# Performance work log

Hardware: AMD Instinct MI355X
Metric: run time of the kernel (lower is better)

Reference implementation:

```python
import jax, jax.numpy as jnp
import numpy as np
import math

B, S, D, H, F = 4, 1024, 1024, 16, 4096
NUM_BUCKETS, MAX_DISTANCE = 32, 128
LN_EPS = 1e-5


def _relative_position_bucket(relative_position, num_buckets=NUM_BUCKETS, max_distance=MAX_DISTANCE):
    # bidirectional T5 bucketing, faithful to the torch source
    n = -relative_position
    num_buckets = num_buckets // 2  # 16
    ret = (n < 0).astype(jnp.int32) * num_buckets
    n = jnp.abs(n)
    max_exact = num_buckets // 2  # 8
    is_small = n < max_exact
    val_if_large = max_exact + (
        jnp.log(jnp.maximum(n, 1).astype(jnp.float32) / max_exact)
        / math.log(max_distance / max_exact)
        * (num_buckets - max_exact)
    ).astype(jnp.int32)
    val_if_large = jnp.minimum(val_if_large, num_buckets - 1)
    return ret + jnp.where(is_small, n, val_if_large)


def layer_norm(x, g, b):
    mu = jnp.mean(x, axis=-1, keepdims=True)
    var = jnp.mean((x - mu) ** 2, axis=-1, keepdims=True)
    return g * (x - mu) / jnp.sqrt(var + LN_EPS) + b


def setup_inputs() -> dict:
    key = jax.random.key(0)
    ks = jax.random.split(key, 12)
    s = 0.02
    return {
        "in_state": jax.random.normal(ks[0], (B, S, D), jnp.float32),
        "padding_mask": jnp.ones((B, S), jnp.int32),
        "Wq": jax.random.normal(ks[1], (D, D), jnp.float32) * s,
        "bq": jnp.zeros((D,), jnp.float32),
        "Wk": jax.random.normal(ks[2], (D, D), jnp.float32) * s,
        "bk": jnp.zeros((D,), jnp.float32),
        "Wv": jax.random.normal(ks[3], (D, D), jnp.float32) * s,
        "bv": jnp.zeros((D,), jnp.float32),
        "Wo": jax.random.normal(ks[4], (D, D), jnp.float32) * s,
        "bo": jnp.zeros((D,), jnp.float32),
        "rel_bias": jax.random.normal(ks[5], (NUM_BUCKETS, H), jnp.float32) * s,
        "ln1_g": jnp.ones((D,), jnp.float32),
        "ln1_b": jnp.zeros((D,), jnp.float32),
        "W1": jax.random.normal(ks[6], (D, F), jnp.float32) * s,
        "b1": jnp.zeros((F,), jnp.float32),
        "W2": jax.random.normal(ks[7], (F, D), jnp.float32) * s,
        "b2": jnp.zeros((D,), jnp.float32),
        "ln2_g": jnp.ones((D,), jnp.float32),
        "ln2_b": jnp.zeros((D,), jnp.float32),
    }


def reference(in_state, padding_mask, Wq, bq, Wk, bk, Wv, bv, Wo, bo, rel_bias,
              ln1_g, ln1_b, W1, b1, W2, b2, ln2_g, ln2_b):
    b, s, d = in_state.shape
    dh = d // H
    q = in_state @ Wq + bq
    k = in_state @ Wk + bk
    v = in_state @ Wv + bv
    # faithful to torch's q.view(B*H, S, d_head) flat reshape (no head transpose)
    qh = q.reshape(b * H, s, dh)
    kh = k.reshape(b * H, s, dh)
    vh = v.reshape(b * H, s, dh)
    scores = jnp.einsum('bqd,bkd->bqk', qh, kh)  # no 1/sqrt(d) scaling (T5 style)
    # relative position bias: [H, S, S] tiled over batch -> block index b*H+h gets head h
    rel_pos = jnp.arange(s)[:, None] - jnp.arange(s)[None, :]
    buckets = _relative_position_bucket(rel_pos)
    bias = rel_bias[buckets].transpose(2, 0, 1)  # [H, S, S]
    bias = jnp.tile(bias, (b, 1, 1))  # [B*H, S, S]
    # padding mask: log(0/1) -> -inf/0; block b*H+h uses mask[b, value_index]
    pad = jnp.log(padding_mask.astype(jnp.float32))  # [B, S]
    pad = jnp.repeat(pad, H, axis=0)[:, None, :]  # [B*H, 1, S]
    attw = jax.nn.softmax(scores + bias + pad, axis=-1)
    att = (attw @ vh).reshape(b, s, d)
    att = att @ Wo + bo
    h = layer_norm(att + in_state, ln1_g, ln1_b)
    ff = jnp.maximum(h @ W1 + b1, 0.0) @ W2 + b2
    out = layer_norm(ff + h, ln2_g, ln2_b)
    return out
```

## Files before the change

### kernel.cpp

```cpp
#include <hip/hip_runtime.h>
#include <hip/hip_bf16.h>

typedef unsigned short u16;
typedef __attribute__((ext_vector_type(8))) short bhalf8;
typedef __attribute__((ext_vector_type(4))) float f32x4;

#define DEV __device__ __forceinline__

DEV float bf2f(u16 u) { union { unsigned int i; float f; } c; c.i = ((unsigned int)u) << 16; return c.f; }
DEV u16 f2bf(float f) {
  union { float f; unsigned int i; } c; c.f = f;
  unsigned int x = c.i;
  x += 0x7fffu + ((x >> 16) & 1u);
  return (u16)(x >> 16);
}

DEV void async16(const void* g, void* l) {
  __builtin_amdgcn_global_load_lds((__attribute__((address_space(1))) void*)g,
                                   (__attribute__((address_space(3))) void*)l, 16, 0, 0);
}

struct Ptr11 { const void* p[11]; };
struct TC4 { const void* in[4]; u16* out[4]; };

__global__ void detect_kernel(const unsigned int* __restrict__ x, int* __restrict__ flag) {
  int t = threadIdx.x;
  int cnt = 0;
  for (int i = t; i < 256; i += 64) {
    unsigned int w = x[i];
    int e = (w >> 7) & 0xFF;
    if (e >= 96 && e <= 134) cnt++;
  }
#pragma unroll
  for (int o = 1; o < 64; o <<= 1) cnt += __shfl_xor(cnt, o, 64);
  if (t == 0) *flag = (cnt >= 192) ? 1 : 0;
}

DEV bhalf8 load8B(const void* base, size_t e, int isbf) {
  if (isbf) return *(const bhalf8*)((const u16*)base + e);
  const float* f = (const float*)base + e;
  float4 a = *(const float4*)f;
  float4 b = *(const float4*)(f + 4);
  bhalf8 r;
  r[0] = (short)f2bf(a.x); r[1] = (short)f2bf(a.y); r[2] = (short)f2bf(a.z); r[3] = (short)f2bf(a.w);
  r[4] = (short)f2bf(b.x); r[5] = (short)f2bf(b.y); r[6] = (short)f2bf(b.z); r[7] = (short)f2bf(b.w);
  return r;
}

__global__ __launch_bounds__(256) void convert_x(const void* __restrict__ x,
                                                 u16* __restrict__ dst,
                                                 const int* __restrict__ flag) {
  int c = blockIdx.x * 256 + threadIdx.x;
  u16* d = dst + (size_t)c * 4;
  if (*flag) {
    *(ushort4*)d = ((const ushort4*)x)[c];
  } else {
    float4 v = ((const float4*)x)[c];
    d[0] = f2bf(v.x); d[1] = f2bf(v.y); d[2] = f2bf(v.z); d[3] = f2bf(v.w);
  }
}

__global__ __launch_bounds__(256) void convert_small(Ptr11 s, float* __restrict__ dst,
                                                     const int* __restrict__ flag) {
  const int isbf = *flag;
  const int SZ[11] = {1024,1024,1024,1024,512,1024,1024,4096,1024,1024,1024};
  for (int i = threadIdx.x; i < 13824; i += 256) {
    int acc = 0, seg = -1, off = 0;
#pragma unroll
    for (int s2 = 0; s2 < 11; ++s2) {
      if (seg < 0 && i < acc + SZ[s2]) { seg = s2; off = i - acc; }
      acc += SZ[s2];
    }
    dst[i] = isbf ? bf2f(((const u16*)s.p[seg])[off]) : ((const float*)s.p[seg])[off];
  }
}

DEV void tconv_tile(const void* in, u16* out, int R, int C, int isbf) {
  __shared__ __align__(16) u16 tile[64][72];
  const int t = threadIdx.x;
  const int c0 = blockIdx.x * 64, r0 = blockIdx.y * 64;
#pragma unroll
  for (int r = 0; r < 2; ++r) {
    int idx = r * 256 + t;
    int ri = idx >> 3, cc = (idx & 7) * 8;
    bhalf8 v = load8B(in, (size_t)(r0 + ri) * C + c0 + cc, isbf);
    *(bhalf8*)(&tile[ri][cc]) = v;
  }
  __syncthreads();
#pragma unroll
  for (int r = 0; r < 2; ++r) {
    int idx = r * 256 + t;
    int co = idx >> 3, rc = (idx & 7) * 8;
    bhalf8 v;
#pragma unroll
    for (int ii = 0; ii < 8; ++ii) v[ii] = (short)tile[rc + ii][co];
    *(bhalf8*)(out + (size_t)(c0 + co) * R + r0 + rc) = v;
  }
}

__global__ __launch_bounds__(256) void tconv_w4(TC4 p, const int* __restrict__ flag) {
  int z = blockIdx.z;
  tconv_tile(p.in[z], p.out[z], 1024, 1024, *flag);
}

__global__ __launch_bounds__(256) void tconv_generic(const void* in, u16* out, int R, int C,
                                                     const int* __restrict__ flag) {
  tconv_tile(in, out, R, C, *flag);
}

__global__ __launch_bounds__(256) void transpose_generic(const u16* in, u16* out, int R, int C) {
  __shared__ __align__(16) u16 tile[64][72];
  const int t = threadIdx.x;
  const int c0 = blockIdx.x * 64, r0 = blockIdx.y * 64;
  size_t bs = (size_t)R * C * blockIdx.z;
#pragma unroll
  for (int r = 0; r < 2; ++r) {
    int idx = r * 256 + t;
    int ri = idx >> 3, cc = (idx & 7) * 8;
    *(bhalf8*)(&tile[ri][cc]) = *(const bhalf8*)(in + bs + (size_t)(r0 + ri) * C + c0 + cc);
  }
  __syncthreads();
#pragma unroll
  for (int r = 0; r < 2; ++r) {
    int idx = r * 256 + t;
    int co = idx >> 3, rc = (idx & 7) * 8;
    bhalf8 v;
#pragma unroll
    for (int ii = 0; ii < 8; ++ii) v[ii] = (short)tile[rc + ii][co];
    *(bhalf8*)(out + bs + (size_t)(c0 + co) * R + r0 + rc) = v;
  }
}

template<int BN, int RELU>
__global__ __launch_bounds__(256) void gemm_bt(
    const u16* __restrict__ A, const u16* __restrict__ BT0,
    const float* __restrict__ b0, const float* __restrict__ b1, const float* __restrict__ b2,
    u16* __restrict__ C0, int M, int N, int K, long sBT, long sC)
{
  constexpr int NFRAG = BN / 32;
  constexpr int BSLOT = BN * 4 / 256;
  __shared__ __align__(16) u16 ldsA[128 * 32];
  __shared__ __align__(16) u16 ldsB[BN * 32];

  const int t = threadIdx.x;
  const int wv = t >> 6, l = t & 63;
  const int wm = wv & 1, wn = wv >> 1;
  const int m0 = blockIdx.y * 128, n0 = blockIdx.x * BN;
  const int z = blockIdx.z;

  const u16* BT = BT0 + (long)z * sBT;
  const float* bias = (z == 0) ? b0 : (z == 1 ? b1 : b2);
  u16* C = C0 + (long)z * sC;

  const u16* agp[2];
#pragma unroll
  for (int r = 0; r < 2; ++r) {
    int s = r * 256 + t;
    int mm = s >> 2, c = (s & 3) ^ ((s >> 4) & 3);
    agp[r] = A + (size_t)(m0 + mm) * K + c * 8;
  }
  const u16* bgp[BSLOT];
#pragma unroll
  for (int r = 0; r < BSLOT; ++r) {
    int s = r * 256 + t;
    int mm = s >> 2, c = (s & 3) ^ ((s >> 4) & 3);
    bgp[r] = BT + (size_t)(n0 + mm) * K + c * 8;
  }

  int a_off[4], b_off[NFRAG];
#pragma unroll
  for (int i = 0; i < 4; ++i) {
    int mm = wm * 64 + i * 16 + (l & 15);
    a_off[i] = (mm * 4 + ((l >> 4) ^ ((mm >> 2) & 3))) * 8;
  }
#pragma unroll
  for (int j = 0; j < NFRAG; ++j) {
    int nn = wn * (BN / 2) + j * 16 + (l & 15);
    b_off[j] = (nn * 4 + ((l >> 4) ^ ((nn >> 2) & 3))) * 8;
  }

  f32x4 acc[4][NFRAG] = {};

  for (int kt = 0; kt < K; kt += 32) {
    __syncthreads();
#pragma unroll
    for (int r = 0; r < 2; ++r)
      async16(agp[r] + kt, (char*)ldsA + r * 4096 + wv * 1024);
#pragma unroll
    for (int r = 0; r < BSLOT; ++r)
      async16(bgp[r] + kt, (char*)ldsB + r * 4096 + wv * 1024);
    __syncthreads();

    bhalf8 af[4], bfr[NFRAG];
#pragma unroll
    for (int i = 0; i < 4; ++i) af[i] = *(const bhalf8*)(ldsA + a_off[i]);
#pragma unroll
    for (int j = 0; j < NFRAG; ++j) bfr[j] = *(const bhalf8*)(ldsB + b_off[j]);
#pragma unroll
    for (int mi = 0; mi < 4; ++mi)
#pragma unroll
      for (int nj = 0; nj < NFRAG; ++nj)
        acc[mi][nj] = __builtin_amdgcn_mfma_f32_16x16x32_bf16(af[mi], bfr[nj], acc[mi][nj], 0, 0, 0);
  }

  const int lr = (l >> 4) << 2, lc = l & 15;
#pragma unroll
  for (int nj = 0; nj < NFRAG; ++nj) {
    int col = n0 + wn * (BN / 2) + nj * 16 + lc;
    float bb = bias[col];
#pragma unroll
    for (int mi = 0; mi < 4; ++mi) {
#pragma unroll
      for (int r = 0; r < 4; ++r) {
        int row = m0 + wm * 64 + mi * 16 + lr + r;
        float v = acc[mi][nj][r] + bb;
        if (RELU) v = fmaxf(v, 0.0f);
        C[(size_t)row * N + col] = f2bf(v);
      }
    }
  }
}

template<int RELU>
__global__ __launch_bounds__(256) void gemm_bn(
    const u16* __restrict__ A, const void* __restrict__ B,
    const float* __restrict__ bias, u16* __restrict__ C, int M, int N, int K,
    const int* __restrict__ flag)
{
  __shared__ __align__(16) u16 ldsA[128][40];
  __shared__ __align__(16) u16 ldsB[128][40];

  const int isbf = *flag;
  const int t = threadIdx.x;
  const int wv = t >> 6, l = t & 63;
  const int wm = wv & 1, wn = wv >> 1;
  const int m0 = blockIdx.y * 128, n0 = blockIdx.x * 128;

  const int srow = t >> 1, scol = (t & 1) * 16;
  const u16* agp = A + (size_t)(m0 + srow) * K + scol;

  const int kk = t >> 3;
  const int nn = (t & 7) * 16;

  f32x4 acc[4][4] = {};

  for (int kt = 0; kt < K; kt += 32) {
    bhalf8 a0 = *(const bhalf8*)(agp + kt);
    bhalf8 a1 = *(const bhalf8*)(agp + kt + 8);
    size_t e0 = (size_t)(kt + kk) * N + n0 + nn;
    bhalf8 b0v = load8B(B, e0, isbf);
    bhalf8 b1v = load8B(B, e0 + 8, isbf);
    __syncthreads();
    *(bhalf8*)(&ldsA[srow][scol])     = a0;
    *(bhalf8*)(&ldsA[srow][scol + 8]) = a1;
#pragma unroll
    for (int j = 0; j < 8; ++j) ldsB[nn + j][kk]     = (u16)b0v[j];
#pragma unroll
    for (int j = 0; j < 8; ++j) ldsB[nn + 8 + j][kk] = (u16)b1v[j];
    __syncthreads();

    bhalf8 af[4], bfr[4];
#pragma unroll
    for (int i = 0; i < 4; ++i)
      af[i] = *(const bhalf8*)(&ldsA[wm * 64 + i * 16 + (l & 15)][(l >> 4) * 8]);
#pragma unroll
    for (int i = 0; i < 4; ++i)
      bfr[i] = *(const bhalf8*)(&ldsB[wn * 64 + i * 16 + (l & 15)][(l >> 4) * 8]);
#pragma unroll
    for (int mi = 0; mi < 4; ++mi)
#pragma unroll
      for (int ni = 0; ni < 4; ++ni)
        acc[mi][ni] = __builtin_amdgcn_mfma_f32_16x16x32_bf16(af[mi], bfr[ni], acc[mi][ni], 0, 0, 0);
  }

  const int lr = (l >> 4) << 2, lc = l & 15;
#pragma unroll
  for (int ni = 0; ni < 4; ++ni) {
    int col = n0 + wn * 64 + ni * 16 + lc;
    float bb = bias[col];
#pragma unroll
    for (int mi = 0; mi < 4; ++mi) {
#pragma unroll
      for (int r = 0; r < 4; ++r) {
        int row = m0 + wm * 64 + mi * 16 + lr + r;
        float v = acc[mi][ni][r] + bb;
        if (RELU) v = fmaxf(v, 0.0f);
        C[(size_t)row * N + col] = f2bf(v);
      }
    }
  }
}

__global__ __launch_bounds__(256) void lut_kernel(const float* __restrict__ rbc, float* __restrict__ lut) {
  int idx = blockIdx.x * 256 + threadIdx.x;
  if (idx >= 16 * 2047) return;
  int h = idx / 2047;
  int dp = idx - h * 2047;
  int delta = dp - 1023;
  int n = -delta;
  int ret = 0;
  if (n < 0) { ret = 16; n = -n; }
  int bkt;
  if (n < 8) bkt = n;
  else {
    float v = logf((float)n * 0.125f) / logf(16.0f) * 8.0f;
    bkt = 8 + (int)v;
    if (bkt > 15) bkt = 15;
  }
  lut[idx] = (rbc[(ret + bkt) * 16 + h] - 12.0f) * 1.44269504f;
}

__global__ __launch_bounds__(256) void attn_fused(
    const u16* __restrict__ q, const u16* __restrict__ k, const u16* __restrict__ vt,
    const int* __restrict__ mask, const float* __restrict__ lut, u16* __restrict__ att)
{
  __shared__ __align__(16) u16 ldsQ[64][72];
  __shared__ __align__(16) u16 ldsK[64][72];
  __shared__ __align__(16) u16 ldsV[64][72];
  __shared__ __align__(16) u16 ldsP[4][16][72];
  __shared__ float ldsLut[2047];
  __shared__ float ldsPad[64];

  const int t = threadIdx.x;
  const int wv = t >> 6, l = t & 63;
  const int bh = blockIdx.x, qt = blockIdx.y;
  const int b = bh >> 4, h = bh & 15;
  const size_t base = (size_t)bh * 65536;
  const int q0 = qt * 64;

  for (int i = t; i < 2047; i += 256) ldsLut[i] = lut[h * 2047 + i];

  const int sr = t >> 2, sc = (t & 3) * 16;
  {
    bhalf8 q0v = *(const bhalf8*)(q + base + (size_t)(q0 + sr) * 64 + sc);
    bhalf8 q1v = *(const bhalf8*)(q + base + (size_t)(q0 + sr) * 64 + sc + 8);
    *(bhalf8*)(&ldsQ[sr][sc])     = q0v;
    *(bhalf8*)(&ldsQ[sr][sc + 8]) = q1v;
  }
  __syncthreads();

  bhalf8 qf[2];
  {
    int mm = wv * 16 + (l & 15);
#pragma unroll
    for (int s = 0; s < 2; ++s)
      qf[s] = *(const bhalf8*)(&ldsQ[mm][s * 32 + (l >> 4) * 8]);
  }

  float ls_part[4] = {0.0f, 0.0f, 0.0f, 0.0f};
  f32x4 acc_o[4] = {};

  const int* mrow = mask + b * 1024;

  for (int kt = 0; kt < 16; ++kt) {
    const int k0 = kt * 64;
    bhalf8 k0v = *(const bhalf8*)(k + base + (size_t)(k0 + sr) * 64 + sc);
    bhalf8 k1v = *(const bhalf8*)(k + base + (size_t)(k0 + sr) * 64 + sc + 8);
    bhalf8 v0v = *(const bhalf8*)(vt + base + (size_t)sr * 1024 + k0 + sc);
    bhalf8 v1v = *(const bhalf8*)(vt + base + (size_t)sr * 1024 + k0 + sc + 8);
    __syncthreads();
    *(bhalf8*)(&ldsK[sr][sc])     = k0v;
    *(bhalf8*)(&ldsK[sr][sc + 8]) = k1v;
    *(bhalf8*)(&ldsV[sr][sc])     = v0v;
    *(bhalf8*)(&ldsV[sr][sc + 8]) = v1v;
    if (t < 64) {
      int mv = mrow[k0 + t];
      ldsPad[t] = (mv > 0) ? __log2f((float)mv) : -1e30f;
    }
    __syncthreads();

    f32x4 accS[4] = {};
#pragma unroll
    for (int s = 0; s < 2; ++s) {
#pragma unroll
      for (int ni = 0; ni < 4; ++ni) {
        int nnj = ni * 16 + (l & 15);
        bhalf8 kf = *(const bhalf8*)(&ldsK[nnj][s * 32 + (l >> 4) * 8]);
        accS[ni] = __builtin_amdgcn_mfma_f32_16x16x32_bf16(qf[s], kf, accS[ni], 0, 0, 0);
      }
    }

    float padv[4];
#pragma unroll
    for (int ni = 0; ni < 4; ++ni) padv[ni] = ldsPad[ni * 16 + (l & 15)];
    const int ib = q0 + wv * 16 + ((l >> 4) << 2);
#pragma unroll
    for (int r = 0; r < 4; ++r) {
      int i_l = ((l >> 4) << 2) + r;
#pragma unroll
      for (int ni = 0; ni < 4; ++ni) {
        int j_l = ni * 16 + (l & 15);
        float s = fmaf(accS[ni][r], 1.44269504f, ldsLut[(ib + r) - (k0 + j_l) + 1023]) + padv[ni];
        float p = exp2f(s);
        ls_part[r] += p;
        ldsP[wv][i_l][j_l] = f2bf(p);
      }
    }

#pragma unroll
    for (int s = 0; s < 2; ++s) {
      int mm = l & 15;
      bhalf8 pf = *(const bhalf8*)(&ldsP[wv][mm][s * 32 + (l >> 4) * 8]);
#pragma unroll
      for (int ni = 0; ni < 4; ++ni) {
        int e = ni * 16 + (l & 15);
        bhalf8 vf = *(const bhalf8*)(&ldsV[e][s * 32 + (l >> 4) * 8]);
        acc_o[ni] = __builtin_amdgcn_mfma_f32_16x16x32_bf16(pf, vf, acc_o[ni], 0, 0, 0);
      }
    }
  }

#pragma unroll
  for (int r = 0; r < 4; ++r) {
#pragma unroll
    for (int off = 1; off < 16; off <<= 1) ls_part[r] += __shfl_xor(ls_part[r], off, 64);
    ls_part[r] = 1.0f / ls_part[r];
  }

#pragma unroll
  for (int ni = 0; ni < 4; ++ni) {
#pragma unroll
    for (int r = 0; r < 4; ++r) {
      int i = q0 + wv * 16 + ((l >> 4) << 2) + r;
      int e = ni * 16 + (l & 15);
      att[base + (size_t)i * 64 + e] = f2bf(acc_o[ni][r] * ls_part[r]);
    }
  }
}

template<int LAST>
__global__ __launch_bounds__(256) void ln_kernel(
    const u16* __restrict__ x, const u16* __restrict__ res,
    const float* __restrict__ g, const float* __restrict__ b,
    void* __restrict__ out, const int* __restrict__ flag)
{
  const int row = blockIdx.x, t = threadIdx.x;
  const size_t off = (size_t)row * 1024 + t * 4;
  ushort4 xv = *(const ushort4*)(x + off);
  ushort4 rv = *(const ushort4*)(res + off);
  float v0 = bf2f(xv.x) + bf2f(rv.x);
  float v1 = bf2f(xv.y) + bf2f(rv.y);
  float v2 = bf2f(xv.z) + bf2f(rv.z);
  float v3 = bf2f(xv.w) + bf2f(rv.w);
  float s = v0 + v1 + v2 + v3;
  float sq = v0 * v0 + v1 * v1 + v2 * v2 + v3 * v3;
#pragma unroll
  for (int o = 1; o < 64; o <<= 1) { s += __shfl_xor(s, o, 64); sq += __shfl_xor(sq, o, 64); }
  __shared__ float red[8];
  const int wv = t >> 6, l = t & 63;
  if (l == 0) { red[wv] = s; red[4 + wv] = sq; }
  __syncthreads();
  s = red[0] + red[1] + red[2] + red[3];
  sq = red[4] + red[5] + red[6] + red[7];
  float mu = s * 0.0009765625f;
  float var = sq * 0.0009765625f - mu * mu;
  float rstd = rsqrtf(var + 1e-5f);
  float4 gv = *(const float4*)(g + t * 4);
  float4 bv = *(const float4*)(b + t * 4);
  float o0 = gv.x * (v0 - mu) * rstd + bv.x;
  float o1 = gv.y * (v1 - mu) * rstd + bv.y;
  float o2 = gv.z * (v2 - mu) * rstd + bv.z;
  float o3 = gv.w * (v3 - mu) * rstd + bv.w;
  if (!LAST) {
    ushort4 ov; ov.x = f2bf(o0); ov.y = f2bf(o1); ov.z = f2bf(o2); ov.w = f2bf(o3);
    *(ushort4*)((u16*)out + off) = ov;
  } else {
    if (*flag) {
      ushort4 ov; ov.x = f2bf(o0); ov.y = f2bf(o1); ov.z = f2bf(o2); ov.w = f2bf(o3);
      *(ushort4*)((u16*)out + off) = ov;
    } else {
      float4 ov; ov.x = o0; ov.y = o1; ov.z = o2; ov.w = o3;
      *(float4*)((float*)out + off) = ov;
    }
  }
}

extern "C" void kernel_launch(void* const* d_in, const int* in_sizes, int n_in,
                              void* d_out, int out_size, void* d_ws, size_t ws_size,
                              hipStream_t stream) {
  const void* x  = d_in[0];
  const int* mask = (const int*)d_in[1];
  const void* Wq = d_in[2];  const void* bq = d_in[3];
  const void* Wk = d_in[4];  const void* bk = d_in[5];
  const void* Wv = d_in[6];  const void* bv = d_in[7];
  const void* Wo = d_in[8];  const void* bo = d_in[9];
  const void* rb = d_in[10];
  const void* g1 = d_in[11]; const void* be1 = d_in[12];
  const void* W1 = d_in[13]; const void* b1 = d_in[14];
  const void* W2 = d_in[15]; const void* b2 = d_in[16];
  const void* g2 = d_in[17]; const void* be2 = d_in[18];

  char* ws = (char*)d_ws;
  const size_t MB = 1024 * 1024;
  const bool FAST = (ws_size >= 57 * MB);

  const size_t TAIL = FAST ? 56 * MB : 48 * MB;
  float* smalls = (float*)(ws + TAIL);
  float* lut    = (float*)(ws + TAIL + 56 * 1024);
  int*   flag   = (int*)(ws + TAIL + 192 * 1024);

  float* bqc  = smalls + 0;
  float* bkc  = smalls + 1024;
  float* bvc  = smalls + 2048;
  float* boc  = smalls + 3072;
  float* rbc  = smalls + 4096;
  float* g1c  = smalls + 4608;
  float* be1c = smalls + 5632;
  float* b1c  = smalls + 6656;
  float* b2c  = smalls + 10752;
  float* g2c  = smalls + 11776;
  float* be2c = smalls + 12800;

  detect_kernel<<<1, 64, 0, stream>>>((const unsigned int*)x, flag);
  Ptr11 sml;
  sml.p[0] = bq; sml.p[1] = bk; sml.p[2] = bv; sml.p[3] = bo; sml.p[4] = rb;
  sml.p[5] = g1; sml.p[6] = be1; sml.p[7] = b1; sml.p[8] = b2; sml.p[9] = g2; sml.p[10] = be2;
  convert_small<<<1, 256, 0, stream>>>(sml, smalls, flag);
  lut_kernel<<<dim3(128), 256, 0, stream>>>(rbc, lut);

  if (FAST) {
    u16* xc   = (u16*)(ws + 0 * MB);
    u16* WqT  = (u16*)(ws + 8 * MB);
    u16* WkT  = WqT + 1048576;
    u16* WvT  = WqT + 2 * 1048576;
    u16* WoT  = WqT + 3 * 1048576;
    u16* qb   = (u16*)(ws + 16 * MB);
    u16* kb   = (u16*)(ws + 24 * MB);
    u16* vb   = (u16*)(ws + 32 * MB);
    u16* vtb  = (u16*)(ws + 40 * MB);
    u16* attb = (u16*)(ws + 32 * MB);
    u16* xo   = (u16*)(ws + 16 * MB);
    u16* hb   = (u16*)(ws + 48 * MB);
    u16* W1T  = (u16*)(ws + 8 * MB);
    u16* W2T  = (u16*)(ws + 0 * MB);
    u16* ff1  = (u16*)(ws + 16 * MB);
    u16* ff2o = (u16*)(ws + 8 * MB);

    convert_x<<<4096, 256, 0, stream>>>(x, xc, flag);
    TC4 tw; tw.in[0] = Wq; tw.in[1] = Wk; tw.in[2] = Wv; tw.in[3] = Wo;
    tw.out[0] = WqT; tw.out[1] = WkT; tw.out[2] = WvT; tw.out[3] = WoT;
    tconv_w4<<<dim3(16, 16, 4), 256, 0, stream>>>(tw, flag);

    gemm_bt<64, 0><<<dim3(16, 32, 3), 256, 0, stream>>>(xc, WqT, bqc, bkc, bvc, qb,
                                                        4096, 1024, 1024, 1048576L, 4194304L);
    transpose_generic<<<dim3(1, 16, 64), 256, 0, stream>>>(vb, vtb, 1024, 64);
    attn_fused<<<dim3(64, 16), 256, 0, stream>>>(qb, kb, vtb, mask, lut, attb);
    gemm_bt<64, 0><<<dim3(16, 32, 1), 256, 0, stream>>>(attb, WoT, boc, boc, boc, xo,
                                                        4096, 1024, 1024, 0L, 0L);
    tconv_generic<<<dim3(64, 16), 256, 0, stream>>>(W1, W1T, 1024, 4096, flag);
    ln_kernel<0><<<dim3(4096), 256, 0, stream>>>(xo, xc, g1c, be1c, hb, flag);
    tconv_generic<<<dim3(16, 64), 256, 0, stream>>>(W2, W2T, 4096, 1024, flag);
    gemm_bt<128, 1><<<dim3(32, 32, 1), 256, 0, stream>>>(hb, W1T, b1c, b1c, b1c, ff1,
                                                         4096, 4096, 1024, 0L, 0L);
    gemm_bt<64, 0><<<dim3(16, 32, 1), 256, 0, stream>>>(ff1, W2T, b2c, b2c, b2c, ff2o,
                                                        4096, 1024, 4096, 0L, 0L);
    ln_kernel<1><<<dim3(4096), 256, 0, stream>>>(ff2o, hb, g2c, be2c, d_out, flag);
  } else {
    u16* xc   = (u16*)(ws + 0 * MB);
    u16* WqT  = (u16*)(ws + 8 * MB);
    u16* WkT  = WqT + 1048576;
    u16* WvT  = WqT + 2 * 1048576;
    u16* WoT  = WqT + 3 * 1048576;
    u16* qb   = (u16*)(ws + 16 * MB);
    u16* kb   = (u16*)(ws + 24 * MB);
    u16* vb   = (u16*)(ws + 32 * MB);
    u16* vtb  = (u16*)(ws + 40 * MB);
    u16* attb = (u16*)(ws + 32 * MB);
    u16* xo   = (u16*)(ws + 16 * MB);
    u16* hb   = (u16*)(ws + 40 * MB);
    u16* ff1  = (u16*)(ws + 0 * MB);
    u16* ff2o = (u16*)(ws + 32 * MB);

    convert_x<<<4096, 256, 0, stream>>>(x, xc, flag);
    TC4 tw; tw.in[0] = Wq; tw.in[1] = Wk; tw.in[2] = Wv; tw.in[3] = Wo;
    tw.out[0] = WqT; tw.out[1] = WkT; tw.out[2] = WvT; tw.out[3] = WoT;
    tconv_w4<<<dim3(16, 16, 4), 256, 0, stream>>>(tw, flag);

    gemm_bt<64, 0><<<dim3(16, 32, 3), 256, 0, stream>>>(xc, WqT, bqc, bkc, bvc, qb,
                                                        4096, 1024, 1024, 1048576L, 4194304L);
    transpose_generic<<<dim3(1, 16, 64), 256, 0, stream>>>(vb, vtb, 1024, 64);
    attn_fused<<<dim3(64, 16), 256, 0, stream>>>(qb, kb, vtb, mask, lut, attb);
    gemm_bt<64, 0><<<dim3(16, 32, 1), 256, 0, stream>>>(attb, WoT, boc, boc, boc, xo,
                                                        4096, 1024, 1024, 0L, 0L);
    ln_kernel<0><<<dim3(4096), 256, 0, stream>>>(xo, xc, g1c, be1c, hb, flag);
    gemm_bn<1><<<dim3(32, 32), 256, 0, stream>>>(hb, W1, b1c, ff1, 4096, 4096, 1024, flag);
    gemm_bn<0><<<dim3(8, 32), 256, 0, stream>>>(ff1, W2, b2c, ff2o, 4096, 1024, 4096, flag);
    ln_kernel<1><<<dim3(4096), 256, 0, stream>>>(ff2o, hb, g2c, be2c, d_out, flag);
  }
}
```

Baseline: 469.8 us.

## Double-buffer LDS tiles in bf16 GEMM to overlap global loads with MFMA

The GEMM main loop now uses two LDS buffers per operand and prefetches the next K-tile with async global-to-LDS loads while the current tile is computed. Explicit s_waitcnt on vmcnt replaces the full __syncthreads pair, so each iteration waits only for the previous tile's loads. The aim is to hide global memory latency behind the MFMA work, at the cost of doubled LDS per block (possible occupancy loss). It also relies on hand-coded waitcnt encodings being correct for the number of outstanding loads.

```diff
diff --git a/kernel.cpp b/kernel.cpp
--- a/kernel.cpp
+++ b/kernel.cpp
@@ -139,8 +139,12 @@
 {
   constexpr int NFRAG = BN / 32;
   constexpr int BSLOT = BN * 4 / 256;
-  __shared__ __align__(16) u16 ldsA[128 * 32];
-  __shared__ __align__(16) u16 ldsB[BN * 32];
+  constexpr int P = 2 + BSLOT;
+  constexpr int WAIT_P = 0xF70 | P;
+  constexpr int WAIT_0 = 0xF70;
+
+  __shared__ __align__(16) u16 ldsA[2][128 * 32];
+  __shared__ __align__(16) u16 ldsB[2][BN * 32];
 
   const int t = threadIdx.x;
   const int wv = t >> 6, l = t & 63;
@@ -181,21 +185,36 @@
 
   f32x4 acc[4][NFRAG] = {};
 
-  for (int kt = 0; kt < K; kt += 32) {
-    __syncthreads();
-#pragma unroll
-    for (int r = 0; r < 2; ++r)
-      async16(agp[r] + kt, (char*)ldsA + r * 4096 + wv * 1024);
-#pragma unroll
-    for (int r = 0; r < BSLOT; ++r)
-      async16(bgp[r] + kt, (char*)ldsB + r * 4096 + wv * 1024);
-    __syncthreads();
+#pragma unroll
+  for (int r = 0; r < 2; ++r)
+    async16(agp[r], (char*)(&ldsA[0][0]) + r * 4096 + wv * 1024);
+#pragma unroll
+  for (int r = 0; r < BSLOT; ++r)
+    async16(bgp[r], (char*)(&ldsB[0][0]) + r * 4096 + wv * 1024);
+
+  const int nT = K >> 5;
+  for (int kt = 0; kt < nT; ++kt) {
+    const int cur = kt & 1;
+    __builtin_amdgcn_s_barrier();
+    if (kt + 1 < nT) {
+      const int koff = (kt + 1) << 5;
+#pragma unroll
+      for (int r = 0; r < 2; ++r)
+        async16(agp[r] + koff, (char*)(&ldsA[cur ^ 1][0]) + r * 4096 + wv * 1024);
+#pragma unroll
+      for (int r = 0; r < BSLOT; ++r)
+        async16(bgp[r] + koff, (char*)(&ldsB[cur ^ 1][0]) + r * 4096 + wv * 1024);
+      __builtin_amdgcn_s_waitcnt(WAIT_P);
+    } else {
+      __builtin_amdgcn_s_waitcnt(WAIT_0);
+    }
+    __builtin_amdgcn_s_barrier();
 
     bhalf8 af[4], bfr[NFRAG];
 #pragma unroll
-    for (int i = 0; i < 4; ++i) af[i] = *(const bhalf8*)(ldsA + a_off[i]);
-#pragma unroll
-    for (int j = 0; j < NFRAG; ++j) bfr[j] = *(const bhalf8*)(ldsB + b_off[j]);
+    for (int i = 0; i < 4; ++i) af[i] = *(const bhalf8*)(&ldsA[cur][0] + a_off[i]);
+#pragma unroll
+    for (int j = 0; j < NFRAG; ++j) bfr[j] = *(const bhalf8*)(&ldsB[cur][0] + b_off[j]);
 #pragma unroll
     for (int mi = 0; mi < 4; ++mi)
 #pragma unroll
```

Result: faster. 455.1 us (-3.1%).
